# Kernel tuning notes

Measured on AMD Instinct MI355X. Metric: run time of the kernel, lower is better.

## Reference

```python
import jax, jax.numpy as jnp
import numpy as np

N_F = 256
D = 4 * N_F          # d_model after PixelUnshuffle(2)
D_INNER = 2 * D      # mamba expand=2
D_STATE = 16
DT_RANK = D // 16
N_LAYERS = 8
BATCH = 16
IMG = 32


def _pixel_unshuffle(x, r):
    b, c, h, w = x.shape
    x = x.reshape(b, c, h // r, r, w // r, r)
    return x.transpose(0, 1, 3, 5, 2, 4).reshape(b, c * r * r, h // r, w // r)


def _pixel_shuffle(x, r):
    b, c, h, w = x.shape
    co = c // (r * r)
    x = x.reshape(b, co, r, r, h, w)
    return x.transpose(0, 1, 4, 2, 5, 3).reshape(b, co, h * r, w * r)


def _layernorm(x, w, b):
    mu = jnp.mean(x, -1, keepdims=True)
    var = jnp.mean((x - mu) ** 2, -1, keepdims=True)
    return (x - mu) * jax.lax.rsqrt(var + 1e-5) * w + b


def _transpose_xy(a):
    b, l, c = a.shape
    s = int(np.sqrt(l))
    return a.reshape(b, s, s, c).transpose(0, 2, 1, 3).reshape(b, l, c)


def _mamba_mixer(u, W_in_i, conv_w_i, conv_b_i, W_x_i, W_dt_i, b_dt_i, A_log_i, D_skip_i, W_out_i):
    b, l, d = u.shape
    xz = jnp.einsum('bld,ed->ble', u, W_in_i)          # (B,L,2*d_inner)
    x, z = jnp.split(xz, 2, axis=-1)
    # causal depthwise conv over sequence, kernel 4, left-pad 3
    xt = jax.lax.conv_general_dilated(
        x.transpose(0, 2, 1), conv_w_i[:, None, :], (1,), [(3, 0)],
        feature_group_count=D_INNER, dimension_numbers=('NCH', 'OIH', 'NCH'))
    x = jax.nn.silu((xt + conv_b_i[None, :, None]).transpose(0, 2, 1))  # (B,L,d_inner)
    dbc = jnp.einsum('ble,fe->blf', x, W_x_i)          # (B,L,dt_rank+2*d_state)
    dt = jax.nn.softplus(jnp.einsum('blr,er->ble', dbc[..., :DT_RANK], W_dt_i) + b_dt_i)
    Bm = dbc[..., DT_RANK:DT_RANK + D_STATE]
    Cm = dbc[..., DT_RANK + D_STATE:]
    A = -jnp.exp(A_log_i)                              # (d_inner, d_state)

    def step(h, inp):
        dt_t, B_t, C_t, x_t = inp                      # (B,di),(B,ds),(B,ds),(B,di)
        h = jnp.exp(dt_t[..., None] * A) * h + (dt_t * x_t)[..., None] * B_t[:, None, :]
        return h, jnp.einsum('bds,bs->bd', h, C_t)

    h0 = jnp.zeros((b, D_INNER, D_STATE), dtype=u.dtype)
    _, ys = jax.lax.scan(step, h0, (dt.transpose(1, 0, 2), Bm.transpose(1, 0, 2),
                                    Cm.transpose(1, 0, 2), x.transpose(1, 0, 2)))
    y = ys.transpose(1, 0, 2) + x * D_skip_i
    y = y * jax.nn.silu(z)
    return jnp.einsum('ble,de->bld', y, W_out_i)


def setup_inputs() -> dict:
    key = jax.random.key(0)
    ks = jax.random.split(key, 20)
    s = 0.02
    inp = {
        'x': jax.random.normal(ks[0], (BATCH, 3, IMG, IMG), jnp.float32),
        'noise_level': jax.random.uniform(ks[1], (BATCH, 1, 1, 1), jnp.float32),
        'pe_w1': jax.random.normal(ks[2], (N_F, 4), jnp.float32) * s,
        'pe_b1': jnp.zeros((N_F,), jnp.float32),
        'pe_w2': jax.random.normal(ks[3], (N_F, N_F), jnp.float32) * s,
        'ln_w': jnp.ones((N_LAYERS, D), jnp.float32),
        'ln_b': jnp.zeros((N_LAYERS, D), jnp.float32),
        'W_in': jax.random.normal(ks[4], (N_LAYERS, 2 * D_INNER, D), jnp.float32) * s,
        'conv_w': jax.random.normal(ks[5], (N_LAYERS, D_INNER, 4), jnp.float32) * s,
        'conv_b': jnp.zeros((N_LAYERS, D_INNER), jnp.float32),
        'W_x': jax.random.normal(ks[6], (N_LAYERS, DT_RANK + 2 * D_STATE, D_INNER), jnp.float32) * s,
        'W_dt': jax.random.normal(ks[7], (N_LAYERS, D_INNER, DT_RANK), jnp.float32) * s,
        'b_dt': jax.random.normal(ks[8], (N_LAYERS, D_INNER), jnp.float32) * s,
        'A_log': jnp.broadcast_to(jnp.log(jnp.arange(1, D_STATE + 1, dtype=jnp.float32)),
                                  (N_LAYERS, D_INNER, D_STATE)),
        'D_skip': jnp.ones((N_LAYERS, D_INNER), jnp.float32),
        'W_out': jax.random.normal(ks[9], (N_LAYERS, D, D_INNER), jnp.float32) * s,
        'op_w1': jax.random.normal(ks[10], (4 * N_F, 12 * N_F), jnp.float32) * s,
        'op_b1': jnp.zeros((4 * N_F,), jnp.float32),
        'op_w2': jax.random.normal(ks[11], (3, N_F), jnp.float32) * s,
        'op_b2': jnp.zeros((3,), jnp.float32),
    }
    return inp


def reference(x, noise_level, pe_w1, pe_b1, pe_w2, ln_w, ln_b, W_in, conv_w, conv_b,
              W_x, W_dt, b_dt, A_log, D_skip, W_out, op_w1, op_b1, op_w2, op_b2):
    B, _, H, W = x.shape
    nl = jnp.broadcast_to(noise_level, (B, 1, H, W))
    h = jnp.concatenate([x, nl], axis=1)                       # (B,4,H,W)
    h = jax.nn.relu(jnp.einsum('bchw,oc->bohw', h, pe_w1) + pe_b1[None, :, None, None])
    h = jnp.einsum('bchw,oc->bohw', h, pe_w2)
    X = _pixel_unshuffle(h, 2)                                 # (B,4*n_f,H/2,W/2)
    Bc, C, Hh, Ww = X.shape
    y = X.reshape(Bc, C, Hh * Ww).transpose(0, 2, 1)           # (B,L,d_model)
    z = None
    for i in range(N_LAYERS):
        z = y if z is None else y + z                          # Block residual routing
        yn = _layernorm(z, ln_w[i], ln_b[i])
        y = _mamba_mixer(yn, W_in[i], conv_w[i], conv_b[i], W_x[i], W_dt[i], b_dt[i],
                         A_log[i], D_skip[i], W_out[i])
        y = _transpose_xy(y)
        z = _transpose_xy(z)
        if (i + 1) % 4 == 0:
            y = y[:, ::-1]
            z = z[:, ::-1]
    y2 = y.transpose(0, 2, 1).reshape(X.shape)
    z2 = z.transpose(0, 2, 1).reshape(X.shape)
    out = jnp.concatenate([X, y2, z2], axis=1)                 # (B,12*n_f,H/2,W/2)
    out = jax.nn.relu(jnp.einsum('bchw,oc->bohw', out, op_w1) + op_b1[None, :, None, None])
    out = _pixel_shuffle(out, 2)                               # (B,n_f,H,W)
    out = jnp.einsum('bchw,oc->bohw', out, op_w2) + op_b2[None, :, None, None]
    return out
```

## Files before the change

kernel.cpp:

```cpp
#include <hip/hip_runtime.h>

typedef unsigned short u16;
typedef __bf16 bf16x8 __attribute__((ext_vector_type(8)));
typedef float f32x4 __attribute__((ext_vector_type(4)));
typedef const __attribute__((address_space(1))) void* as1p;
typedef __attribute__((address_space(3))) void* as3p;

#define VMCNT4 asm volatile("s_waitcnt vmcnt(4)" ::: "memory")
#define VMCNT2 asm volatile("s_waitcnt vmcnt(2)" ::: "memory")
#define VMCNT0 asm volatile("s_waitcnt vmcnt(0)" ::: "memory")
#define LGKM0  asm volatile("s_waitcnt lgkmcnt(0)" ::: "memory")

__device__ __forceinline__ float bf2f(u16 h) { return __uint_as_float(((unsigned)h) << 16); }
__device__ __forceinline__ float ldf(const void* p, size_t i, int bf) {
    return bf ? bf2f(((const u16*)p)[i]) : ((const float*)p)[i];
}
__device__ __forceinline__ float4 ldf4(const void* p, size_t i, int bf) {
    if (bf) {
        const u16* q = (const u16*)p + i;
        ushort4 v = *(const ushort4*)q;
        return make_float4(bf2f(v.x), bf2f(v.y), bf2f(v.z), bf2f(v.w));
    }
    return *(const float4*)((const float*)p + i);
}
__device__ __forceinline__ u16 f2bf(float f) {
    unsigned u = __float_as_uint(f);
    unsigned r = (u + 0x7FFFu + ((u >> 16) & 1u)) >> 16;
    return (u16)r;
}
__device__ __forceinline__ float silu_f(float x) { return x * (1.f / (1.f + __expf(-x))); }

__device__ __forceinline__ int permL(int l, int rev) {
    if (rev) l = 255 - l;
    return ((l & 15) << 4) | (l >> 4);
}

__device__ __forceinline__ void gload_lds16(const void* g, void* l) {
    __builtin_amdgcn_global_load_lds((as1p)g, (as3p)l, 16, 0, 0);
}

__global__ void k_detect(const void* lnw, int* flag) {
    if (threadIdx.x == 0 && blockIdx.x == 0) {
        unsigned w = ((const unsigned*)lnw)[0];
        *flag = (w == 0x3F803F80u) ? 1 : 0;
    }
}

__global__ void k_cvt(const void* src, size_t soff, u16* __restrict__ dst, int n,
                      const int* __restrict__ flagp) {
    int bf = *flagp;
    int i4 = (blockIdx.x * 256 + threadIdx.x) * 4;
    if (i4 >= n) return;
    float4 v = ldf4(src, soff + i4, bf);
    *(ushort4*)(dst + i4) = make_ushort4(f2bf(v.x), f2bf(v.y), f2bf(v.z), f2bf(v.w));
}

__global__ void k_cvt_padx(const void* src, u16* __restrict__ dst,
                           const int* __restrict__ flagp) {
    int bf = *flagp;
    int i4 = (blockIdx.x * 256 + threadIdx.x) * 4;
    int row = i4 >> 11, col = i4 & 2047;
    int layer = row >> 7, lrow = row & 127;
    ushort4 o = make_ushort4(0, 0, 0, 0);
    if (lrow < 96) {
        float4 v = ldf4(src, (size_t)layer * 96 * 2048 + (size_t)lrow * 2048 + col, bf);
        o = make_ushort4(f2bf(v.x), f2bf(v.y), f2bf(v.z), f2bf(v.w));
    }
    *(ushort4*)(dst + i4) = o;
}

__global__ void k_head1(const void* x, const void* nl, const void* w1, const void* b1,
                        float* __restrict__ h1, const int* flagp) {
    int bf = *flagp;
    int idx = blockIdx.x * 256 + threadIdx.x;
    int o = idx & 255, p = (idx >> 8) & 1023, b = idx >> 18;
    float c0 = ldf(x, ((size_t)b * 3 + 0) * 1024 + p, bf);
    float c1 = ldf(x, ((size_t)b * 3 + 1) * 1024 + p, bf);
    float c2 = ldf(x, ((size_t)b * 3 + 2) * 1024 + p, bf);
    float c3 = ldf(nl, b, bf);
    float acc = ldf(w1, (size_t)o * 4 + 0, bf) * c0 + ldf(w1, (size_t)o * 4 + 1, bf) * c1 +
                ldf(w1, (size_t)o * 4 + 2, bf) * c2 + ldf(w1, (size_t)o * 4 + 3, bf) * c3 +
                ldf(b1, o, bf);
    h1[idx] = fmaxf(acc, 0.f);
}

template <int EPI>
__global__ __launch_bounds__(256) void k_gemm(
    const float* __restrict__ A, int lda,
    const void* __restrict__ W, size_t woff,
    const void* __restrict__ bias, size_t boff,
    float* __restrict__ C, int N, int K,
    const int* __restrict__ flagp, int perm) {
    int bf = *flagp;
    __shared__ float As[16][68];
    __shared__ float Ws[16][68];
    int t = threadIdx.x;
    int m0 = blockIdx.y * 64, n0 = blockIdx.x * 64;
    int lrow = t >> 2, lcol = (t & 3) << 2;
    int tx = t & 15, tyr = t >> 4;
    float acc[4][4] = {};
    for (int k0 = 0; k0 < K; k0 += 16) {
        float4 av = *(const float4*)(A + (size_t)(m0 + lrow) * lda + k0 + lcol);
        float4 wv = make_float4(0.f, 0.f, 0.f, 0.f);
        int nrow = n0 + lrow;
        if (nrow < N) wv = ldf4(W, woff + (size_t)nrow * K + k0 + lcol, bf);
        __syncthreads();
        As[lcol + 0][lrow] = av.x; As[lcol + 1][lrow] = av.y;
        As[lcol + 2][lrow] = av.z; As[lcol + 3][lrow] = av.w;
        Ws[lcol + 0][lrow] = wv.x; Ws[lcol + 1][lrow] = wv.y;
        Ws[lcol + 2][lrow] = wv.z; Ws[lcol + 3][lrow] = wv.w;
        __syncthreads();
#pragma unroll
        for (int k = 0; k < 16; ++k) {
            float4 a = *(const float4*)&As[k][tyr << 2];
            float4 bv = *(const float4*)&Ws[k][tx << 2];
            float aa[4] = {a.x, a.y, a.z, a.w};
            float bb[4] = {bv.x, bv.y, bv.z, bv.w};
#pragma unroll
            for (int i = 0; i < 4; ++i)
#pragma unroll
                for (int j = 0; j < 4; ++j) acc[i][j] += aa[i] * bb[j];
        }
    }
#pragma unroll
    for (int i = 0; i < 4; ++i) {
        int m = m0 + (tyr << 2) + i;
        int mo = m;
        if (perm >= 0) { int b = m >> 8, l = m & 255; mo = (b << 8) | permL(l, perm); }
#pragma unroll
        for (int j = 0; j < 4; ++j) {
            int n = n0 + (tx << 2) + j;
            if (n >= N) continue;
            float v = acc[i][j];
            if (EPI == 1) { v += ldf(bias, boff + n, bf); v = fmaxf(v, 0.f); }
            if (EPI == 2) { v += ldf(bias, boff + n, bf); v = (v > 20.f) ? v : log1pf(expf(v)); }
            C[(size_t)mo * N + n] = v;
        }
    }
}

template <int MODE>
__global__ __launch_bounds__(512, 2) void k_m256(
    const u16* __restrict__ A, int lda,
    const u16* __restrict__ W, int ldw,
    void* __restrict__ Cv, int ldc, int ktPerZ,
    const void* cw, size_t cwo, const void* cb, size_t cbo,
    u16* __restrict__ xc16, u16* __restrict__ z16,
    const int* __restrict__ flagp) {
    __shared__ __align__(16) u16 lds[65536];
    int t = threadIdx.x;
    int w = t >> 6, lane = t & 63;
    int wm = w >> 2, wn = w & 3;
    int fr = lane & 15, q = lane >> 4;
    int flat = blockIdx.y * gridDim.x + blockIdx.x;
    int nwg = gridDim.x * gridDim.y, cpx = nwg >> 3;
    int tid = (flat & 7) * cpx + (flat >> 3);
    int bx = tid % gridDim.x, by = tid / gridDim.x;
    int m0 = by * 256, n0 = bx * 256;
    int kt0 = blockIdx.z * ktPerZ;
    int sr = t >> 3, sslot = t & 7;

    auto stA = [&](int d, int kt, int h, int j) {
        int lr = j * 64 + sr;
        int gr = (lr >> 6) * 128 + h * 64 + (lr & 63);
        int col = kt * 64 + ((sslot ^ (lr & 7)) << 3);
        gload_lds16(A + (size_t)(m0 + gr) * lda + col,
                    &lds[(d * 2 + h) * 8192 + lr * 64 + sslot * 8]);
    };
    auto stB = [&](int d, int kt, int h, int j) {
        int lr = j * 64 + sr;
        int gr = (lr >> 5) * 64 + h * 32 + (lr & 31);
        int col = kt * 64 + ((sslot ^ (lr & 7)) << 3);
        gload_lds16(W + (size_t)(n0 + gr) * ldw + col,
                    &lds[32768 + (d * 2 + h) * 8192 + lr * 64 + sslot * 8]);
    };
    auto ldA = [&](int d, int mf, int kk) {
        int lr = wm * 64 + (mf & 3) * 16 + fr;
        int sl = (kk * 4 + q) ^ (lr & 7);
        return *(const bf16x8*)&lds[(d * 2 + (mf >> 2)) * 8192 + lr * 64 + sl * 8];
    };
    auto ldB = [&](int d, int nf, int kk) {
        int lr = wn * 32 + (nf & 1) * 16 + fr;
        int sl = (kk * 4 + q) ^ (lr & 7);
        return *(const bf16x8*)&lds[32768 + (d * 2 + (nf >> 1)) * 8192 + lr * 64 + sl * 8];
    };

    f32x4 acc[8][4] = {};
    bf16x8 av[4][2], bv0[2][2], bv1[2][2];

    stA(0, kt0, 0, 0); stA(0, kt0, 0, 1); stA(0, kt0, 1, 0); stA(0, kt0, 1, 1);
    stB(0, kt0, 0, 0); stB(0, kt0, 0, 1); stB(0, kt0, 1, 0); stB(0, kt0, 1, 1);
    VMCNT0;
    __builtin_amdgcn_s_barrier();

    for (int kt = kt0; kt < kt0 + ktPerZ; ++kt) {
        int d = (kt - kt0) & 1, nd = d ^ 1, nk = kt + 1;
        bool more = nk < kt0 + ktPerZ;
        VMCNT4;
        __builtin_amdgcn_s_barrier();
        if (more) { stA(nd, nk, 0, 0); stA(nd, nk, 0, 1); }
#pragma unroll
        for (int m = 0; m < 4; ++m) { av[m][0] = ldA(d, m, 0); av[m][1] = ldA(d, m, 1); }
#pragma unroll
        for (int n = 0; n < 2; ++n) { bv0[n][0] = ldB(d, n, 0); bv0[n][1] = ldB(d, n, 1); }
        LGKM0; __builtin_amdgcn_sched_barrier(0);
        __builtin_amdgcn_s_setprio(1);
#pragma unroll
        for (int m = 0; m < 4; ++m)
#pragma unroll
            for (int n = 0; n < 2; ++n) {
                acc[m][n] = __builtin_amdgcn_mfma_f32_16x16x32_bf16(av[m][0], bv0[n][0], acc[m][n], 0, 0, 0);
                acc[m][n] = __builtin_amdgcn_mfma_f32_16x16x32_bf16(av[m][1], bv0[n][1], acc[m][n], 0, 0, 0);
            }
        __builtin_amdgcn_s_setprio(0);
        if (more) { VMCNT4; } else { VMCNT2; }
        __builtin_amdgcn_s_barrier();
        if (more) { stB(nd, nk, 0, 0); stB(nd, nk, 0, 1); }
#pragma unroll
        for (int n = 0; n < 2; ++n) { bv1[n][0] = ldB(d, n + 2, 0); bv1[n][1] = ldB(d, n + 2, 1); }
        LGKM0; __builtin_amdgcn_sched_barrier(0);
        __builtin_amdgcn_s_setprio(1);
#pragma unroll
        for (int m = 0; m < 4; ++m)
#pragma unroll
            for (int n = 0; n < 2; ++n) {
                acc[m][n + 2] = __builtin_amdgcn_mfma_f32_16x16x32_bf16(av[m][0], bv1[n][0], acc[m][n + 2], 0, 0, 0);
                acc[m][n + 2] = __builtin_amdgcn_mfma_f32_16x16x32_bf16(av[m][1], bv1[n][1], acc[m][n + 2], 0, 0, 0);
            }
        __builtin_amdgcn_s_setprio(0);
        if (more) { VMCNT4; } else { VMCNT0; }
        __builtin_amdgcn_s_barrier();
        if (more) { stB(nd, nk, 1, 0); stB(nd, nk, 1, 1); }
#pragma unroll
        for (int m = 0; m < 4; ++m) { av[m][0] = ldA(d, m + 4, 0); av[m][1] = ldA(d, m + 4, 1); }
        LGKM0; __builtin_amdgcn_sched_barrier(0);
        __builtin_amdgcn_s_setprio(1);
#pragma unroll
        for (int m = 0; m < 4; ++m)
#pragma unroll
            for (int n = 0; n < 2; ++n) {
                acc[m + 4][n] = __builtin_amdgcn_mfma_f32_16x16x32_bf16(av[m][0], bv0[n][0], acc[m + 4][n], 0, 0, 0);
                acc[m + 4][n] = __builtin_amdgcn_mfma_f32_16x16x32_bf16(av[m][1], bv0[n][1], acc[m + 4][n], 0, 0, 0);
            }
        __builtin_amdgcn_s_setprio(0);
        VMCNT4;
        __builtin_amdgcn_s_barrier();
        if (more) { stA(nd, nk, 1, 0); stA(nd, nk, 1, 1); }
        __builtin_amdgcn_s_setprio(1);
#pragma unroll
        for (int m = 0; m < 4; ++m)
#pragma unroll
            for (int n = 0; n < 2; ++n) {
                acc[m + 4][n + 2] = __builtin_amdgcn_mfma_f32_16x16x32_bf16(av[m][0], bv1[n][0], acc[m + 4][n + 2], 0, 0, 0);
                acc[m + 4][n + 2] = __builtin_amdgcn_mfma_f32_16x16x32_bf16(av[m][1], bv1[n][1], acc[m + 4][n + 2], 0, 0, 0);
            }
        __builtin_amdgcn_s_setprio(0);
    }

    if (MODE == 0) {
        float* Cf = (float*)Cv + (size_t)blockIdx.z * (size_t)gridDim.y * 256 * ldc;
#pragma unroll
        for (int m = 0; m < 8; ++m) {
            int row = m0 + wm * 128 + m * 16 + q * 4;
#pragma unroll
            for (int rr = 0; rr < 4; ++rr)
#pragma unroll
                for (int n = 0; n < 4; ++n)
                    Cf[(size_t)(row + rr) * ldc + n0 + wn * 64 + n * 16 + fr] = acc[m][n][rr];
        }
    } else {
        int bf = *flagp;
        if (n0 < 2048) {
            __syncthreads();
#pragma unroll
            for (int m = 0; m < 8; ++m) {
                int row = wm * 128 + m * 16 + q * 4;
#pragma unroll
                for (int rr = 0; rr < 4; ++rr) {
                    int r = row + rr, xo = ((r >> 2) & 3) << 4;
#pragma unroll
                    for (int n = 0; n < 4; ++n) {
                        int c = wn * 64 + n * 16 + fr;
                        lds[r * 256 + (c ^ xo)] = f2bf(acc[m][n][rr]);
                    }
                }
            }
            __syncthreads();
            int col = t & 255, half = t >> 8;
            int c = n0 + col;
            float w0 = ldf(cw, cwo + (size_t)c * 4 + 0, bf);
            float w1 = ldf(cw, cwo + (size_t)c * 4 + 1, bf);
            float w2 = ldf(cw, cwo + (size_t)c * 4 + 2, bf);
            float w3 = ldf(cw, cwo + (size_t)c * 4 + 3, bf);
            float cbv = ldf(cb, cbo + c, bf);
            int l0 = half * 128;
            float x1 = 0.f, x2 = 0.f, x3 = 0.f;
            if (l0) {
                x1 = bf2f(lds[(l0 - 1) * 256 + (col ^ ((((l0 - 1) >> 2) & 3) << 4))]);
                x2 = bf2f(lds[(l0 - 2) * 256 + (col ^ ((((l0 - 2) >> 2) & 3) << 4))]);
                x3 = bf2f(lds[(l0 - 3) * 256 + (col ^ ((((l0 - 3) >> 2) & 3) << 4))]);
            }
            for (int r = 0; r < 128; ++r) {
                int l = l0 + r;
                float xv = bf2f(lds[l * 256 + (col ^ (((l >> 2) & 3) << 4))]);
                float a = cbv + w3 * xv + w2 * x1 + w1 * x2 + w0 * x3;
                xc16[(size_t)(m0 + l) * 2048 + c] = f2bf(silu_f(a));
                x3 = x2; x2 = x1; x1 = xv;
            }
        } else {
            int cb0 = n0 - 2048;
#pragma unroll
            for (int m = 0; m < 8; ++m) {
                int row = m0 + wm * 128 + m * 16 + q * 4;
#pragma unroll
                for (int rr = 0; rr < 4; ++rr)
#pragma unroll
                    for (int n = 0; n < 4; ++n)
                        z16[(size_t)(row + rr) * 2048 + cb0 + wn * 64 + n * 16 + fr] =
                            f2bf(acc[m][n][rr]);
            }
        }
    }
}

template <int EPI, int OUT16, int BN>
__global__ __launch_bounds__(256) void k_mgemm(
    const u16* __restrict__ A, int lda,
    const u16* __restrict__ W, int ldw,
    const void* __restrict__ bias, size_t boff,
    void* __restrict__ Cv, int ldc, int N,
    int ktPerZ, int perm, const int* __restrict__ flagp) {
    constexpr int NF = BN / 32;
    int bf = *flagp;
    __shared__ __align__(16) u16 As[128 * 32];
    __shared__ __align__(16) u16 Bs[BN * 32];
    int t = threadIdx.x;
    int gx = gridDim.x;
    int flat = blockIdx.y * gx + blockIdx.x;
    int nwg = gx * gridDim.y;
    if ((nwg & 7) == 0) {
        int cpx = nwg >> 3;
        flat = (flat & 7) * cpx + (flat >> 3);
    }
    int bx = flat % gx, by = flat / gx;
    int m0 = by * 128, n0 = bx * BN;
    int kt0 = blockIdx.z * ktPerZ;
    float* Cf = (float*)Cv + (size_t)blockIdx.z * (size_t)gridDim.y * 128 * ldc;
    u16* Ch = (u16*)Cv;
    int w = t >> 6, lane = t & 63;
    int wm = w >> 1, wn = w & 1;
    int fr = lane & 15, kb = (lane >> 4) * 8;
    int srow = lane >> 2, scol = (lane & 3) * 8;
    f32x4 acc[4][NF] = {};
    for (int kt = kt0; kt < kt0 + ktPerZ; ++kt) {
        int kc = kt * 32;
#pragma unroll
        for (int i = 0; i < 2; ++i) {
            int r = i * 64 + w * 16 + srow;
            gload_lds16(A + (size_t)(m0 + r) * lda + kc + scol, As + i * 2048 + w * 512);
        }
#pragma unroll
        for (int i = 0; i < BN / 64; ++i) {
            int r = i * 64 + w * 16 + srow;
            gload_lds16(W + (size_t)(n0 + r) * ldw + kc + scol, Bs + i * 2048 + w * 512);
        }
        __syncthreads();
        bf16x8 af[4], bv[NF];
#pragma unroll
        for (int m = 0; m < 4; ++m)
            af[m] = *(const bf16x8*)(As + (wm * 64 + m * 16 + fr) * 32 + kb);
#pragma unroll
        for (int n = 0; n < NF; ++n)
            bv[n] = *(const bf16x8*)(Bs + (wn * NF * 16 + n * 16 + fr) * 32 + kb);
#pragma unroll
        for (int m = 0; m < 4; ++m)
#pragma unroll
            for (int n = 0; n < NF; ++n)
                acc[m][n] = __builtin_amdgcn_mfma_f32_16x16x32_bf16(af[m], bv[n], acc[m][n], 0, 0, 0);
        __syncthreads();
    }
    int r0 = (lane >> 4) * 4;
#pragma unroll
    for (int m = 0; m < 4; ++m) {
        int rowb = m0 + wm * 64 + m * 16 + r0;
#pragma unroll
        for (int rr = 0; rr < 4; ++rr) {
            int row = rowb + rr;
            int mo = row;
            if (perm >= 0) { int bb = row >> 8, l = row & 255; mo = (bb << 8) | permL(l, perm); }
#pragma unroll
            for (int n = 0; n < NF; ++n) {
                int col = n0 + wn * NF * 16 + n * 16 + fr;
                if (col >= N) continue;
                float v = acc[m][n][rr];
                if (EPI == 1) { v += ldf(bias, boff + col, bf); v = fmaxf(v, 0.f); }
                if (EPI == 2) { v += ldf(bias, boff + col, bf); v = (v > 20.f) ? v : log1pf(expf(v)); }
                if (OUT16) Ch[(size_t)mo * ldc + col] = f2bf(v);
                else       Cf[(size_t)mo * ldc + col] = v;
            }
        }
    }
}

template <int EPI>
__global__ void k_ored(const float* __restrict__ part, float* __restrict__ out,
                       const void* __restrict__ bias,
                       const int* __restrict__ flagp, int perm, int nz) {
    int bf = *flagp;
    int idx4 = (blockIdx.x * 256 + threadIdx.x) * 4;
    int m = idx4 >> 10, n = idx4 & 1023;
    float4 s = make_float4(0.f, 0.f, 0.f, 0.f);
    for (int z = 0; z < nz; ++z) {
        float4 p = *(const float4*)(part + (size_t)z * 4096 * 1024 + (size_t)m * 1024 + n);
        s.x += p.x; s.y += p.y; s.z += p.z; s.w += p.w;
    }
    if (EPI == 1) {
        s.x = fmaxf(s.x + ldf(bias, n + 0, bf), 0.f);
        s.y = fmaxf(s.y + ldf(bias, n + 1, bf), 0.f);
        s.z = fmaxf(s.z + ldf(bias, n + 2, bf), 0.f);
        s.w = fmaxf(s.w + ldf(bias, n + 3, bf), 0.f);
    }
    int mo = m;
    if (perm >= 0) { int b = m >> 8, l = m & 255; mo = (b << 8) | permL(l, perm); }
    *(float4*)(out + (size_t)mo * 1024 + n) = s;
}

__global__ void k_xred(const float* __restrict__ part, float* __restrict__ dbc,
                       u16* __restrict__ dbc16) {
    int idx = blockIdx.x * 256 + threadIdx.x;
    int m = idx / 96, n = idx - m * 96;
    float s = 0.f;
#pragma unroll
    for (int z = 0; z < 8; ++z) s += part[(size_t)z * 4096 * 128 + (size_t)m * 128 + n];
    dbc[idx] = s;
    dbc16[idx] = f2bf(s);
}

__global__ void k_rearr(const float* __restrict__ h2, float* __restrict__ X) {
    int idx = blockIdx.x * 256 + threadIdx.x;
    int d = idx & 1023, l = (idx >> 10) & 255, b = idx >> 18;
    int o = d >> 2, r1 = (d >> 1) & 1, r2 = d & 1;
    int hh = l >> 4, ww = l & 15;
    int p = ((hh << 1) | r1) * 32 + ((ww << 1) | r2);
    X[idx] = h2[((size_t)b * 1024 + p) * 256 + o];
}

__global__ __launch_bounds__(256) void k_lnr(
    const float* __restrict__ yin,
    const float* __restrict__ opart,
    const float* __restrict__ zold,
    float* __restrict__ znew, u16* __restrict__ yn16,
    const void* lnw, const void* lnb, size_t lno,
    const int* __restrict__ flagp, int prevPerm, int first) {
    int bf = *flagp;
    int m = blockIdx.x, b = m >> 8, l = m & 255;
    int t = threadIdx.x;
    float4 v;
    if (first) {
        v = *(const float4*)(yin + (size_t)m * 1024 + (t << 2));
    } else {
        size_t row2 = (size_t)((b << 8) | permL(l, prevPerm)) * 1024 + (t << 2);
        float4 p0 = *(const float4*)(opart + row2);
        float4 p1 = *(const float4*)(opart + 4194304ull + row2);
        float4 p2 = *(const float4*)(opart + 2ull * 4194304 + row2);
        float4 p3 = *(const float4*)(opart + 3ull * 4194304 + row2);
        float4 zv = *(const float4*)(zold + row2);
        v.x = ((p0.x + p1.x) + p2.x) + p3.x + zv.x;
        v.y = ((p0.y + p1.y) + p2.y) + p3.y + zv.y;
        v.z = ((p0.z + p1.z) + p2.z) + p3.z + zv.z;
        v.w = ((p0.w + p1.w) + p2.w) + p3.w + zv.w;
    }
    *(float4*)(znew + (size_t)m * 1024 + (t << 2)) = v;
    float s = v.x + v.y + v.z + v.w;
    float s2 = v.x * v.x + v.y * v.y + v.z * v.z + v.w * v.w;
#pragma unroll
    for (int o = 32; o > 0; o >>= 1) { s += __shfl_down(s, o, 64); s2 += __shfl_down(s2, o, 64); }
    __shared__ float red[8];
    __shared__ float mv[2];
    int wid = t >> 6;
    if ((t & 63) == 0) { red[wid] = s; red[4 + wid] = s2; }
    __syncthreads();
    if (t == 0) {
        float a = red[0] + red[1] + red[2] + red[3];
        float c = red[4] + red[5] + red[6] + red[7];
        float mu = a * (1.f / 1024.f);
        mv[0] = mu;
        mv[1] = rsqrtf(c * (1.f / 1024.f) - mu * mu + 1e-5f);
    }
    __syncthreads();
    float mu = mv[0], rs = mv[1];
    size_t wb = lno + (t << 2);
    float o0 = (v.x - mu) * rs * ldf(lnw, wb + 0, bf) + ldf(lnb, wb + 0, bf);
    float o1 = (v.y - mu) * rs * ldf(lnw, wb + 1, bf) + ldf(lnb, wb + 1, bf);
    float o2 = (v.z - mu) * rs * ldf(lnw, wb + 2, bf) + ldf(lnb, wb + 2, bf);
    float o3 = (v.w - mu) * rs * ldf(lnw, wb + 3, bf) + ldf(lnb, wb + 3, bf);
    *(ushort4*)(yn16 + (size_t)m * 1024 + (t << 2)) =
        make_ushort4(f2bf(o0), f2bf(o1), f2bf(o2), f2bf(o3));
}

__global__ __launch_bounds__(256) void k_scan_a(
    const float* __restrict__ dbc, const float* __restrict__ dt,
    const u16* __restrict__ xc16, const void* A_log, size_t ao,
    float* __restrict__ hsum, float* __restrict__ sumdt,
    const int* __restrict__ flagp) {
    int bf = *flagp;
    __shared__ float Bs[32][16];
    int t = threadIdx.x;
    int bid = blockIdx.x;
    int dg = bid & 7, ch = (bid >> 3) & 7, b = bid >> 6;
    int d = dg * 256 + t, l0 = ch * 32;
    if (t < 128) {
        int l = t >> 2, q = (t & 3) * 4;
        *(float4*)&Bs[l][q] = *(const float4*)(dbc + (size_t)(b * 256 + l0 + l) * 96 + 64 + q);
    }
    float aneg[16];
#pragma unroll
    for (int s = 0; s < 16; ++s) aneg[s] = -__expf(ldf(A_log, ao + (size_t)d * 16 + s, bf));
    float h[16];
#pragma unroll
    for (int s = 0; s < 16; ++s) h[s] = 0.f;
    float sd = 0.f;
    __syncthreads();
    const float* dtp = dt + (size_t)(b * 256 + l0) * 2048 + d;
    const u16* xp = xc16 + (size_t)(b * 256 + l0) * 2048 + d;
#pragma unroll
    for (int half = 0; half < 2; ++half) {
        float dtv[16], xv[16];
#pragma unroll
        for (int j = 0; j < 16; ++j) {
            dtv[j] = dtp[(size_t)(half * 16 + j) * 2048];
            xv[j] = bf2f(xp[(size_t)(half * 16 + j) * 2048]);
        }
#pragma unroll
        for (int j = 0; j < 16; ++j) {
            int l = half * 16 + j;
            float dx = dtv[j] * xv[j];
#pragma unroll
            for (int s = 0; s < 16; ++s) {
                float e = __expf(dtv[j] * aneg[s]);
                h[s] = e * h[s] + dx * Bs[l][s];
            }
            sd += dtv[j];
        }
    }
    size_t base = ((size_t)(b * 8 + ch) * 16) * 2048 + d;
#pragma unroll
    for (int s = 0; s < 16; ++s) hsum[base + (size_t)s * 2048] = h[s];
    sumdt[(size_t)(b * 8 + ch) * 2048 + d] = sd;
}

__global__ __launch_bounds__(256) void k_scan_c(
    const float* __restrict__ dbc, const float* __restrict__ dt,
    const u16* __restrict__ xc16, const u16* __restrict__ z16,
    const float* __restrict__ hsum, const float* __restrict__ sumdt,
    const void* A_log, size_t ao,
    const void* Dsk, size_t doo, u16* __restrict__ ys16,
    const int* __restrict__ flagp) {
    int bf = *flagp;
    __shared__ float Bs[32][16];
    __shared__ float Cs[32][16];
    int t = threadIdx.x;
    int bid = blockIdx.x;
    int dg = bid & 7, ch = (bid >> 3) & 7, b = bid >> 6;
    int d = dg * 256 + t, l0 = ch * 32;
    if (t < 128) {
        int l = t >> 2, q = (t & 3) * 4;
        const float* row = dbc + (size_t)(b * 256 + l0 + l) * 96;
        *(float4*)&Bs[l][q] = *(const float4*)(row + 64 + q);
        *(float4*)&Cs[l][q] = *(const float4*)(row + 80 + q);
    }
    float aneg[16];
#pragma unroll
    for (int s = 0; s < 16; ++s) aneg[s] = -__expf(ldf(A_log, ao + (size_t)d * 16 + s, bf));
    float h[16];
#pragma unroll
    for (int s = 0; s < 16; ++s) h[s] = 0.f;
    for (int c = 0; c < ch; ++c) {
        float sd = sumdt[(size_t)(b * 8 + c) * 2048 + d];
        size_t hb = ((size_t)(b * 8 + c) * 16) * 2048 + d;
#pragma unroll
        for (int s = 0; s < 16; ++s)
            h[s] = __expf(aneg[s] * sd) * h[s] + hsum[hb + (size_t)s * 2048];
    }
    float Dv = ldf(Dsk, doo + d, bf);
    __syncthreads();
    const float* dtp = dt + (size_t)(b * 256 + l0) * 2048 + d;
    const u16* xp = xc16 + (size_t)(b * 256 + l0) * 2048 + d;
    const u16* zp = z16 + (size_t)(b * 256 + l0) * 2048 + d;
    u16* yp = ys16 + (size_t)(b * 256 + l0) * 2048 + d;
#pragma unroll
    for (int half = 0; half < 2; ++half) {
        float dtv[16], xv[16], zv[16];
#pragma unroll
        for (int j = 0; j < 16; ++j) {
            dtv[j] = dtp[(size_t)(half * 16 + j) * 2048];
            xv[j] = bf2f(xp[(size_t)(half * 16 + j) * 2048]);
            zv[j] = bf2f(zp[(size_t)(half * 16 + j) * 2048]);
        }
#pragma unroll
        for (int j = 0; j < 16; ++j) {
            int l = half * 16 + j;
            float dx = dtv[j] * xv[j];
            float acc = 0.f;
#pragma unroll
            for (int s = 0; s < 16; ++s) {
                float e = __expf(dtv[j] * aneg[s]);
                h[s] = e * h[s] + dx * Bs[l][s];
                acc += h[s] * Cs[l][s];
            }
            float v = (acc + xv[j] * Dv) * silu_f(zv[j]);
            yp[(size_t)l * 2048] = f2bf(v);
        }
    }
}

__global__ void k_concat(const float* __restrict__ X, const float* __restrict__ y,
                         const float* __restrict__ z, u16* __restrict__ cat16) {
    int idx = blockIdx.x * 256 + threadIdx.x;
    int c = idx % 3072;
    int m = idx / 3072;
    float v;
    if (c < 1024) v = X[(size_t)m * 1024 + c];
    else if (c < 2048) v = y[(size_t)m * 1024 + (c - 1024)];
    else {
        int b = m >> 8, l = m & 255;
        int l2 = permL(l, 1);
        v = z[((size_t)((b << 8) | l2)) * 1024 + (c - 2048)];
    }
    cat16[idx] = f2bf(v);
}

__global__ void k_final(const float* __restrict__ out1, const void* w2, const void* b2,
                        void* out, const int* __restrict__ flagp) {
    int bf = *flagp;
    int idx = blockIdx.x * 256 + threadIdx.x;
    int j = idx & 31, i = (idx >> 5) & 31, b = idx >> 10;
    int hh = i >> 1, r1 = i & 1, ww = j >> 1, r2 = j & 1;
    int l = (hh << 4) | ww, roff = (r1 << 1) | r2;
    const float* p = out1 + ((size_t)b * 256 + l) * 1024 + roff;
    float a0 = ldf(b2, 0, bf), a1 = ldf(b2, 1, bf), a2 = ldf(b2, 2, bf);
    for (int co = 0; co < 256; ++co) {
        float v = p[co << 2];
        a0 += v * ldf(w2, co, bf);
        a1 += v * ldf(w2, 256 + co, bf);
        a2 += v * ldf(w2, 512 + co, bf);
    }
    size_t o0 = ((size_t)b * 3) * 1024 + (i << 5) + j;
    if (bf) {
        u16* ob = (u16*)out;
        ob[o0] = f2bf(a0); ob[o0 + 1024] = f2bf(a1); ob[o0 + 2048] = f2bf(a2);
    } else {
        float* of = (float*)out;
        of[o0] = a0; of[o0 + 1024] = a1; of[o0 + 2048] = a2;
    }
}

extern "C" void kernel_launch(void* const* d_in, const int* in_sizes, int n_in,
                              void* d_out, int out_size, void* d_ws, size_t ws_size,
                              hipStream_t stream) {
    const void* I_x   = d_in[0];  const void* I_nl  = d_in[1];
    const void* I_pw1 = d_in[2];  const void* I_pb1 = d_in[3];
    const void* I_pw2 = d_in[4];  const void* I_lnw = d_in[5];
    const void* I_lnb = d_in[6];  const void* I_Win = d_in[7];
    const void* I_cw  = d_in[8];  const void* I_cb  = d_in[9];
    const void* I_Wx  = d_in[10]; const void* I_Wdt = d_in[11];
    const void* I_bdt = d_in[12]; const void* I_Alog = d_in[13];
    const void* I_Dsk = d_in[14]; const void* I_Wout = d_in[15];
    const void* I_ow1 = d_in[16]; const void* I_ob1 = d_in[17];
    const void* I_ow2 = d_in[18]; const void* I_ob2 = d_in[19];

    float* ws = (float*)d_ws;
    int* flag = (int*)d_ws;
    size_t off = 64;
    auto alloc = [&](size_t n) { float* p = ws + off; off += n; return p; };
    const size_t MD = 4096ull * 1024;
    float* Xs    = alloc(MD);
    float* y     = alloc(MD);
    float* za    = alloc(MD);
    float* zb    = alloc(MD);
    float* dbc   = alloc(4096ull * 96);
    float* dtb   = alloc(4096ull * 2048);
    float* hsum  = alloc(16ull * 8 * 16 * 2048);
    float* sumdt = alloc(16ull * 8 * 2048);
    float* opart = alloc(4ull * 4096 * 1024);
    u16* z16   = (u16*)alloc(MD);
    u16* yn16  = (u16*)alloc(MD / 2);
    u16* ys16  = (u16*)alloc(MD);
    u16* xc16  = (u16*)alloc(MD);
    u16* dbc16 = (u16*)alloc(4096ull * 96 / 2);
    u16* wWin  = (u16*)alloc(8ull * 4096 * 1024 / 2);
    u16* wWx   = (u16*)alloc(8ull * 128 * 2048 / 2);
    u16* wWdt  = (u16*)alloc(8ull * 2048 * 64 / 2);
    u16* wWout = (u16*)alloc(8ull * 1024 * 2048 / 2);
    u16* wWop  = (u16*)alloc(1024ull * 3072 / 2);
    float* xpart = dtb + 4194304;
    float* h1 = dtb;
    float* out1 = y;
    u16* cat16 = yn16;
    float* h2 = y;
    float* zbufs[2] = {za, zb};

    k_detect<<<1, 64, 0, stream>>>(I_lnw, flag);

    k_cvt<<<32768, 256, 0, stream>>>(I_Win, 0, wWin, 8 * 4096 * 1024, flag);
    k_cvt_padx<<<2048, 256, 0, stream>>>(I_Wx, wWx, flag);
    k_cvt<<<1024, 256, 0, stream>>>(I_Wdt, 0, wWdt, 8 * 2048 * 64, flag);
    k_cvt<<<16384, 256, 0, stream>>>(I_Wout, 0, wWout, 8 * 1024 * 2048, flag);
    k_cvt<<<3072, 256, 0, stream>>>(I_ow1, 0, wWop, 1024 * 3072, flag);

    k_head1<<<16384, 256, 0, stream>>>(I_x, I_nl, I_pw1, I_pb1, h1, flag);
    k_gemm<0><<<dim3(4, 256), 256, 0, stream>>>(h1, 256, I_pw2, 0, nullptr, 0, h2, 256, 256, flag, -1);
    k_rearr<<<16384, 256, 0, stream>>>(h2, Xs);

    for (int i = 0; i < 8; ++i) {
        int rev = (i == 3 || i == 7) ? 1 : 0;
        int prevPerm = (i >= 1) ? ((i - 1 == 3) ? 1 : 0) : 0;
        float* znew = zbufs[i & 1];
        float* zold = zbufs[(i & 1) ^ 1];
        size_t ao = (size_t)i * 2048 * 16;
        k_lnr<<<4096, 256, 0, stream>>>((i == 0) ? Xs : nullptr, opart, zold, znew, yn16,
                                        I_lnw, I_lnb, (size_t)i * 1024, flag, prevPerm, i == 0);
        k_m256<2><<<dim3(16, 16), 512, 0, stream>>>(
            yn16, 1024, wWin + (size_t)i * 4096 * 1024, 1024, nullptr, 0, 16,
            I_cw, (size_t)i * 2048 * 4, I_cb, (size_t)i * 2048, xc16, z16, flag);
        k_mgemm<0, 0, 128><<<dim3(1, 32, 8), 256, 0, stream>>>(
            xc16, 2048, wWx + (size_t)i * 128 * 2048, 2048, nullptr, 0,
            xpart, 128, 128, 8, -1, flag);
        k_xred<<<1536, 256, 0, stream>>>(xpart, dbc, dbc16);
        k_mgemm<2, 0, 128><<<dim3(16, 32), 256, 0, stream>>>(
            dbc16, 96, wWdt + (size_t)i * 2048 * 64, 64, I_bdt, (size_t)i * 2048,
            dtb, 2048, 2048, 2, -1, flag);
        k_scan_a<<<1024, 256, 0, stream>>>(dbc, dtb, xc16, I_Alog, ao, hsum, sumdt, flag);
        k_scan_c<<<1024, 256, 0, stream>>>(dbc, dtb, xc16, z16, hsum, sumdt, I_Alog, ao,
                                           I_Dsk, (size_t)i * 2048, ys16, flag);
        k_m256<0><<<dim3(4, 16, 4), 512, 0, stream>>>(
            ys16, 2048, wWout + (size_t)i * 1024 * 2048, 2048, opart, 1024, 8,
            nullptr, 0, nullptr, 0, nullptr, nullptr, flag);
        if (i == 7)
            k_ored<0><<<4096, 256, 0, stream>>>(opart, y, nullptr, flag, 1, 4);
    }

    k_concat<<<49152, 256, 0, stream>>>(Xs, y, zbufs[1], cat16);
    k_m256<0><<<dim3(4, 16, 4), 512, 0, stream>>>(
        cat16, 3072, wWop, 3072, opart, 1024, 12,
        nullptr, 0, nullptr, 0, nullptr, nullptr, flag);
    k_ored<1><<<4096, 256, 0, stream>>>(opart, out1, I_ob1, flag, -1, 4);
    k_final<<<64, 256, 0, stream>>>(out1, I_ow2, I_ob2, d_out, flag);
}
```

Before: 2.167 ms.

## Use bf16 MFMA GEMM for patch-embed with fused unshuffle, store dt as bf16

The fp32 scalar patch-embed GEMM and the separate rearrange kernel are replaced by the bf16 MFMA GEMM (k_mgemm) with a new epilogue that writes directly in pixel-unshuffled layout. The head activation is written as bf16. The dt projection now outputs bf16, which halves the read traffic for dt in both scan kernels. In exchange, the patch-embed inputs and dt lose precision by being rounded to bf16.

```diff
diff --git a/kernel.cpp b/kernel.cpp
--- a/kernel.cpp
+++ b/kernel.cpp
@@ -70,7 +70,7 @@
 }
 
 __global__ void k_head1(const void* x, const void* nl, const void* w1, const void* b1,
-                        float* __restrict__ h1, const int* flagp) {
+                        u16* __restrict__ h116, const int* flagp) {
     int bf = *flagp;
     int idx = blockIdx.x * 256 + threadIdx.x;
     int o = idx & 255, p = (idx >> 8) & 1023, b = idx >> 18;
@@ -81,62 +81,7 @@
     float acc = ldf(w1, (size_t)o * 4 + 0, bf) * c0 + ldf(w1, (size_t)o * 4 + 1, bf) * c1 +
                 ldf(w1, (size_t)o * 4 + 2, bf) * c2 + ldf(w1, (size_t)o * 4 + 3, bf) * c3 +
                 ldf(b1, o, bf);
-    h1[idx] = fmaxf(acc, 0.f);
-}
-
-template <int EPI>
-__global__ __launch_bounds__(256) void k_gemm(
-    const float* __restrict__ A, int lda,
-    const void* __restrict__ W, size_t woff,
-    const void* __restrict__ bias, size_t boff,
-    float* __restrict__ C, int N, int K,
-    const int* __restrict__ flagp, int perm) {
-    int bf = *flagp;
-    __shared__ float As[16][68];
-    __shared__ float Ws[16][68];
-    int t = threadIdx.x;
-    int m0 = blockIdx.y * 64, n0 = blockIdx.x * 64;
-    int lrow = t >> 2, lcol = (t & 3) << 2;
-    int tx = t & 15, tyr = t >> 4;
-    float acc[4][4] = {};
-    for (int k0 = 0; k0 < K; k0 += 16) {
-        float4 av = *(const float4*)(A + (size_t)(m0 + lrow) * lda + k0 + lcol);
-        float4 wv = make_float4(0.f, 0.f, 0.f, 0.f);
-        int nrow = n0 + lrow;
-        if (nrow < N) wv = ldf4(W, woff + (size_t)nrow * K + k0 + lcol, bf);
-        __syncthreads();
-        As[lcol + 0][lrow] = av.x; As[lcol + 1][lrow] = av.y;
-        As[lcol + 2][lrow] = av.z; As[lcol + 3][lrow] = av.w;
-        Ws[lcol + 0][lrow] = wv.x; Ws[lcol + 1][lrow] = wv.y;
-        Ws[lcol + 2][lrow] = wv.z; Ws[lcol + 3][lrow] = wv.w;
-        __syncthreads();
-#pragma unroll
-        for (int k = 0; k < 16; ++k) {
-            float4 a = *(const float4*)&As[k][tyr << 2];
-            float4 bv = *(const float4*)&Ws[k][tx << 2];
-            float aa[4] = {a.x, a.y, a.z, a.w};
-            float bb[4] = {bv.x, bv.y, bv.z, bv.w};
-#pragma unroll
-            for (int i = 0; i < 4; ++i)
-#pragma unroll
-                for (int j = 0; j < 4; ++j) acc[i][j] += aa[i] * bb[j];
-        }
-    }
-#pragma unroll
-    for (int i = 0; i < 4; ++i) {
-        int m = m0 + (tyr << 2) + i;
-        int mo = m;
-        if (perm >= 0) { int b = m >> 8, l = m & 255; mo = (b << 8) | permL(l, perm); }
-#pragma unroll
-        for (int j = 0; j < 4; ++j) {
-            int n = n0 + (tx << 2) + j;
-            if (n >= N) continue;
-            float v = acc[i][j];
-            if (EPI == 1) { v += ldf(bias, boff + n, bf); v = fmaxf(v, 0.f); }
-            if (EPI == 2) { v += ldf(bias, boff + n, bf); v = (v > 20.f) ? v : log1pf(expf(v)); }
-            C[(size_t)mo * N + n] = v;
-        }
-    }
+    h116[idx] = f2bf(fmaxf(acc, 0.f));
 }
 
 template <int MODE>
@@ -393,6 +338,14 @@
                 int col = n0 + wn * NF * 16 + n * 16 + fr;
                 if (col >= N) continue;
                 float v = acc[m][n][rr];
+                if (EPI == 3) {
+                    int bB = row >> 10, p = row & 1023;
+                    int pi = p >> 5, pj = p & 31;
+                    int l2 = ((pi >> 1) << 4) | (pj >> 1);
+                    int dd = (col << 2) | ((pi & 1) << 1) | (pj & 1);
+                    Cf[(size_t)(((bB << 8) | l2)) * 1024 + dd] = v;
+                    continue;
+                }
                 if (EPI == 1) { v += ldf(bias, boff + col, bf); v = fmaxf(v, 0.f); }
                 if (EPI == 2) { v += ldf(bias, boff + col, bf); v = (v > 20.f) ? v : log1pf(expf(v)); }
                 if (OUT16) Ch[(size_t)mo * ldc + col] = f2bf(v);
@@ -434,15 +387,6 @@
     for (int z = 0; z < 8; ++z) s += part[(size_t)z * 4096 * 128 + (size_t)m * 128 + n];
     dbc[idx] = s;
     dbc16[idx] = f2bf(s);
-}
-
-__global__ void k_rearr(const float* __restrict__ h2, float* __restrict__ X) {
-    int idx = blockIdx.x * 256 + threadIdx.x;
-    int d = idx & 1023, l = (idx >> 10) & 255, b = idx >> 18;
-    int o = d >> 2, r1 = (d >> 1) & 1, r2 = d & 1;
-    int hh = l >> 4, ww = l & 15;
-    int p = ((hh << 1) | r1) * 32 + ((ww << 1) | r2);
-    X[idx] = h2[((size_t)b * 1024 + p) * 256 + o];
 }
 
 __global__ __launch_bounds__(256) void k_lnr(
@@ -499,7 +443,7 @@
 }
 
 __global__ __launch_bounds__(256) void k_scan_a(
-    const float* __restrict__ dbc, const float* __restrict__ dt,
+    const float* __restrict__ dbc, const u16* __restrict__ dt16,
     const u16* __restrict__ xc16, const void* A_log, size_t ao,
     float* __restrict__ hsum, float* __restrict__ sumdt,
     const int* __restrict__ flagp) {
@@ -521,14 +465,14 @@
     for (int s = 0; s < 16; ++s) h[s] = 0.f;
     float sd = 0.f;
     __syncthreads();
-    const float* dtp = dt + (size_t)(b * 256 + l0) * 2048 + d;
+    const u16* dtp = dt16 + (size_t)(b * 256 + l0) * 2048 + d;
     const u16* xp = xc16 + (size_t)(b * 256 + l0) * 2048 + d;
 #pragma unroll
     for (int half = 0; half < 2; ++half) {
         float dtv[16], xv[16];
 #pragma unroll
         for (int j = 0; j < 16; ++j) {
-            dtv[j] = dtp[(size_t)(half * 16 + j) * 2048];
+            dtv[j] = bf2f(dtp[(size_t)(half * 16 + j) * 2048]);
             xv[j] = bf2f(xp[(size_t)(half * 16 + j) * 2048]);
         }
 #pragma unroll
@@ -550,7 +494,7 @@
 }
 
 __global__ __launch_bounds__(256) void k_scan_c(
-    const float* __restrict__ dbc, const float* __restrict__ dt,
+    const float* __restrict__ dbc, const u16* __restrict__ dt16,
     const u16* __restrict__ xc16, const u16* __restrict__ z16,
     const float* __restrict__ hsum, const float* __restrict__ sumdt,
     const void* A_log, size_t ao,
@@ -584,7 +528,7 @@
     }
     float Dv = ldf(Dsk, doo + d, bf);
     __syncthreads();
-    const float* dtp = dt + (size_t)(b * 256 + l0) * 2048 + d;
+    const u16* dtp = dt16 + (size_t)(b * 256 + l0) * 2048 + d;
     const u16* xp = xc16 + (size_t)(b * 256 + l0) * 2048 + d;
     const u16* zp = z16 + (size_t)(b * 256 + l0) * 2048 + d;
     u16* yp = ys16 + (size_t)(b * 256 + l0) * 2048 + d;
@@ -593,7 +537,7 @@
         float dtv[16], xv[16], zv[16];
 #pragma unroll
         for (int j = 0; j < 16; ++j) {
-            dtv[j] = dtp[(size_t)(half * 16 + j) * 2048];
+            dtv[j] = bf2f(dtp[(size_t)(half * 16 + j) * 2048]);
             xv[j] = bf2f(xp[(size_t)(half * 16 + j) * 2048]);
             zv[j] = bf2f(zp[(size_t)(half * 16 + j) * 2048]);
         }
@@ -693,11 +637,12 @@
     u16* wWdt  = (u16*)alloc(8ull * 2048 * 64 / 2);
     u16* wWout = (u16*)alloc(8ull * 1024 * 2048 / 2);
     u16* wWop  = (u16*)alloc(1024ull * 3072 / 2);
+    u16* wPe   = (u16*)alloc(256ull * 256 / 2);
     float* xpart = dtb + 4194304;
-    float* h1 = dtb;
+    u16* dtb16 = (u16*)dtb;
+    u16* h116  = (u16*)dtb;
     float* out1 = y;
     u16* cat16 = yn16;
-    float* h2 = y;
     float* zbufs[2] = {za, zb};
 
     k_detect<<<1, 64, 0, stream>>>(I_lnw, flag);
@@ -707,13 +652,13 @@
     k_cvt<<<1024, 256, 0, stream>>>(I_Wdt, 0, wWdt, 8 * 2048 * 64, flag);
     k_cvt<<<16384, 256, 0, stream>>>(I_Wout, 0, wWout, 8 * 1024 * 2048, flag);
     k_cvt<<<3072, 256, 0, stream>>>(I_ow1, 0, wWop, 1024 * 3072, flag);
-
-    k_head1<<<16384, 256, 0, stream>>>(I_x, I_nl, I_pw1, I_pb1, h1, flag);
-    k_gemm<0><<<dim3(4, 256), 256, 0, stream>>>(h1, 256, I_pw2, 0, nullptr, 0, h2, 256, 256, flag, -1);
-    k_rearr<<<16384, 256, 0, stream>>>(h2, Xs);
+    k_cvt<<<64, 256, 0, stream>>>(I_pw2, 0, wPe, 256 * 256, flag);
+
+    k_head1<<<16384, 256, 0, stream>>>(I_x, I_nl, I_pw1, I_pb1, h116, flag);
+    k_mgemm<3, 0, 128><<<dim3(2, 128), 256, 0, stream>>>(
+        h116, 256, wPe, 256, nullptr, 0, Xs, 1024, 256, 8, -1, flag);
 
     for (int i = 0; i < 8; ++i) {
-        int rev = (i == 3 || i == 7) ? 1 : 0;
         int prevPerm = (i >= 1) ? ((i - 1 == 3) ? 1 : 0) : 0;
         float* znew = zbufs[i & 1];
         float* zold = zbufs[(i & 1) ^ 1];
@@ -727,11 +672,11 @@
             xc16, 2048, wWx + (size_t)i * 128 * 2048, 2048, nullptr, 0,
             xpart, 128, 128, 8, -1, flag);
         k_xred<<<1536, 256, 0, stream>>>(xpart, dbc, dbc16);
-        k_mgemm<2, 0, 128><<<dim3(16, 32), 256, 0, stream>>>(
+        k_mgemm<2, 1, 128><<<dim3(16, 32), 256, 0, stream>>>(
             dbc16, 96, wWdt + (size_t)i * 2048 * 64, 64, I_bdt, (size_t)i * 2048,
-            dtb, 2048, 2048, 2, -1, flag);
-        k_scan_a<<<1024, 256, 0, stream>>>(dbc, dtb, xc16, I_Alog, ao, hsum, sumdt, flag);
-        k_scan_c<<<1024, 256, 0, stream>>>(dbc, dtb, xc16, z16, hsum, sumdt, I_Alog, ao,
+            dtb16, 2048, 2048, 2, -1, flag);
+        k_scan_a<<<1024, 256, 0, stream>>>(dbc, dtb16, xc16, I_Alog, ao, hsum, sumdt, flag);
+        k_scan_c<<<1024, 256, 0, stream>>>(dbc, dtb16, xc16, z16, hsum, sumdt, I_Alog, ao,
                                            I_Dsk, (size_t)i * 2048, ys16, flag);
         k_m256<0><<<dim3(4, 16, 4), 512, 0, stream>>>(
             ys16, 2048, wWout + (size_t)i * 1024 * 2048, 2048, opart, 1024, 8,
```

After: 2.211 ms. 1.02x slower.
